# Kernel optimization log

Measured on AMD Instinct MI355X. Metric: run time of the kernel, lower is better.

Reference implementation:

```python
import jax, jax.numpy as jnp
import numpy as np

N, M, E = 100000, 500, 300000
XS, GS, OUT, HEADS = 100, 100, 100, 2
SLOPE = 0.2
EPS = 1e-12


def l2norm(x, axis):
    n = jnp.linalg.norm(x, axis=axis, keepdims=True)
    return x / jnp.maximum(n, EPS)


def gat_layer(h_ijk, ends, n, W, att):
    # W: [heads*out, in_dim] (no bias); att: [1, heads, out]
    heads, out = att.shape[1], att.shape[2]
    c = (h_ijk @ W.T).reshape(-1, heads, out)               # [E, H, D]
    a = jnp.sum(att * c, axis=2, keepdims=True)             # [E, H, 1]
    e = jnp.exp(-jax.nn.leaky_relu(a, SLOPE))
    denom = jax.ops.segment_sum(e, ends, num_segments=n)    # [n, H, 1]
    alpha = e / denom[ends]                                 # segment softmax (dropout=eval/identity)
    h = jax.ops.segment_sum(alpha * c, ends, num_segments=n)  # [n, H, D]
    h = jax.nn.elu(h)
    h = l2norm(h, axis=2)
    return h.reshape(n, heads * out)


def merge_layer(h_in, h_out, Wi, bi, Wo, bo, Wl, bl):
    hi = h_in @ Wi.T + bi
    ho = h_out @ Wo.T + bo
    lam = jax.nn.sigmoid(jnp.concatenate([hi, ho], axis=1) @ Wl.T + bl)
    h = lam * hi + (1.0 - lam) * ho
    return l2norm(jax.nn.elu(h), axis=1)


def setup_inputs() -> dict:
    key = jax.random.key(0)
    ks = jax.random.split(key, 24)
    D = HEADS * OUT  # 200
    in1 = 2 * XS + GS   # 300
    in2 = 3 * D         # 600
    s = 0.05
    return {
        'edge_idx': jax.random.randint(ks[0], (2, E), 0, N),
        'edge_type': jax.random.randint(ks[1], (E,), 0, M),
        'path_idx': jax.random.randint(ks[2], (2, 8), 0, N),
        'path_type': jax.random.randint(ks[3], (2, 8), 0, M),
        'use_path': 0,
        'x': jax.random.normal(ks[4], (N, XS), jnp.float32),
        'g': jax.random.normal(ks[5], (M, GS), jnp.float32),
        'W_in1': s * jax.random.normal(ks[6], (D, in1), jnp.float32),
        'att_in1': s * jax.random.normal(ks[7], (1, HEADS, OUT), jnp.float32),
        'W_out1': s * jax.random.normal(ks[8], (D, in1), jnp.float32),
        'att_out1': s * jax.random.normal(ks[9], (1, HEADS, OUT), jnp.float32),
        'Wi1': s * jax.random.normal(ks[10], (D, D), jnp.float32), 'bi1': jnp.zeros((D,), jnp.float32),
        'Wo1': s * jax.random.normal(ks[11], (D, D), jnp.float32), 'bo1': jnp.zeros((D,), jnp.float32),
        'Wl1': s * jax.random.normal(ks[12], (1, 2 * D), jnp.float32), 'bl1': jnp.zeros((1,), jnp.float32),
        'Wr': s * jax.random.normal(ks[13], (D, GS), jnp.float32), 'br': jnp.zeros((D,), jnp.float32),
        'Wf': s * jax.random.normal(ks[14], (D, in1), jnp.float32), 'bf': jnp.zeros((D,), jnp.float32),
        'W_in2': s * jax.random.normal(ks[15], (D, in2), jnp.float32),
        'att_in2': s * jax.random.normal(ks[16], (1, 1, D), jnp.float32),
        'W_out2': s * jax.random.normal(ks[17], (D, in2), jnp.float32),
        'att_out2': s * jax.random.normal(ks[18], (1, 1, D), jnp.float32),
        'Wi2': s * jax.random.normal(ks[19], (D, D), jnp.float32), 'bi2': jnp.zeros((D,), jnp.float32),
        'Wo2': s * jax.random.normal(ks[20], (D, D), jnp.float32), 'bo2': jnp.zeros((D,), jnp.float32),
        'Wl2': s * jax.random.normal(ks[21], (1, 2 * D), jnp.float32), 'bl2': jnp.zeros((1,), jnp.float32),
        'W_ent': s * jax.random.normal(ks[22], (D, XS), jnp.float32),
    }


def reference(edge_idx, edge_type, path_idx, path_type, use_path, x, g,
              W_in1, att_in1, W_out1, att_out1, Wi1, bi1, Wo1, bo1, Wl1, bl1,
              Wr, br, Wf, bf,
              W_in2, att_in2, W_out2, att_out2, Wi2, bi2, Wo2, bo2, Wl2, bl2,
              W_ent):
    n, m = x.shape[0], g.shape[0]
    x = l2norm(x, axis=1)  # x_initial is renormalized each forward
    row, col = edge_idx[0], edge_idx[1]
    # hop 1: gather-concat per-edge features [E, 2*XS+GS]
    h_ijk = jnp.concatenate([x[row], x[col], g[edge_type]], axis=1)
    h_in = gat_layer(h_ijk, col, n, W_in1, att_in1)
    h_out = gat_layer(h_ijk, row, n, W_out1, att_out1)
    h = merge_layer(h_in, h_out, Wi1, bi1, Wo1, bo1, Wl1, bl1)
    # relation layer
    g_edges = jax.ops.segment_sum(h_ijk, edge_type, num_segments=m)
    g_edges = jax.nn.elu(l2norm(g_edges, axis=1))
    g_prime = (g @ Wr.T + br) + (g_edges @ Wf.T + bf)
    # hop 2
    h_ijk2 = jnp.concatenate([h[row], h[col], g_prime[edge_type]], axis=1)
    h_in2 = gat_layer(h_ijk2, col, n, W_in2, att_in2)
    h_out2 = gat_layer(h_ijk2, row, n, W_out2, att_out2)
    h = merge_layer(h_in2, h_out2, Wi2, bi2, Wo2, bo2, Wl2, bl2)
    # entity residual layer
    h_prime = x @ W_ent.T + h
    return h_prime
```

## Files before the change

### kernel.cpp

```cpp
#include <hip/hip_runtime.h>
#include <cstddef>
#include <cstdint>

#define WSLOPE 0.2f
#define WEPS 1e-12f

typedef __attribute__((ext_vector_type(8))) short bf16x8;
typedef __attribute__((ext_vector_type(4))) float f32x4;

__device__ __forceinline__ float waveSum(float v) {
#pragma unroll
    for (int off = 32; off > 0; off >>= 1) v += __shfl_xor(v, off, 64);
    return v;
}
__device__ __forceinline__ float rowSum16(float v) {
#pragma unroll
    for (int off = 8; off > 0; off >>= 1) v += __shfl_xor(v, off, 64);
    return v;
}
__device__ __forceinline__ float eluf(float v) { return v > 0.f ? v : expm1f(v); }
__device__ __forceinline__ short f2bf(float f) {
    union { float f; uint32_t u; } v; v.f = f;
    uint32_t r = v.u + 0x7FFF + ((v.u >> 16) & 1);
    return (short)(r >> 16);
}
__device__ __forceinline__ float bf2f(short s) {
    union { uint32_t u; float f; } v; v.u = ((uint32_t)(uint16_t)s) << 16;
    return v.f;
}

__global__ void k_nodeprep(const float* __restrict__ x, float* __restrict__ invn,
                           short* __restrict__ xnb,
                           const float* __restrict__ wai, const float* __restrict__ wao,
                           float* __restrict__ rdi, float* __restrict__ cdi,
                           float* __restrict__ rdo, float* __restrict__ cdo, int N) {
    int wid = blockIdx.x * 4 + (threadIdx.x >> 6);
    int lane = threadIdx.x & 63;
    if (wid >= N) return;
    const float* p = x + (size_t)wid * 100;
    float a0 = p[lane];
    float a1 = (lane < 36) ? p[lane + 64] : 0.f;
    float ss = waveSum(a0 * a0 + a1 * a1);
    float inv = 1.f / fmaxf(sqrtf(ss), WEPS);
    if (lane == 0) invn[wid] = inv;
    float f0 = a0 * inv, f1 = a1 * inv;
    short* xb = xnb + (size_t)wid * 112;
    xb[lane] = f2bf(f0);
    if (lane < 36) xb[64 + lane] = f2bf(f1);
    else if (lane < 48) xb[64 + lane] = 0;
#pragma unroll
    for (int h = 0; h < 2; ++h) {
        const float* wi = wai + h * 300;
        const float* wo = wao + h * 300;
        float ri = f0 * wi[lane] + f1 * wi[lane + 64];
        float ci = f0 * wi[100 + lane] + f1 * wi[100 + lane + 64];
        float ro = f0 * wo[lane] + f1 * wo[lane + 64];
        float co = f0 * wo[100 + lane] + f1 * wo[100 + lane + 64];
        ri = waveSum(ri); ci = waveSum(ci); ro = waveSum(ro); co = waveSum(co);
        if (lane == 0) { rdi[wid * 2 + h] = ri; cdi[wid * 2 + h] = ci; rdo[wid * 2 + h] = ro; cdo[wid * 2 + h] = co; }
    }
}

__global__ void k_gprep(const float* __restrict__ g, short* __restrict__ gbf,
                        short* __restrict__ gcomb,
                        const float* __restrict__ wai, const float* __restrict__ wao,
                        float* __restrict__ gdi, float* __restrict__ gdo, int M) {
    int m = blockIdx.x * 4 + (threadIdx.x >> 6);
    int lane = threadIdx.x & 63;
    if (m >= M) return;
    const float* gm = g + (size_t)m * 100;
    float v0 = gm[lane];
    float v1 = (lane < 36) ? gm[lane + 64] : 0.f;
    short b0 = f2bf(v0), b1 = (lane < 36) ? f2bf(v1) : (short)0;
    short* gb = gbf + (size_t)m * 112;
    gb[lane] = b0;
    if (lane < 48) gb[64 + lane] = (lane < 36) ? b1 : (short)0;
    short* gc = gcomb + (size_t)m * 416;
    gc[lane] = b0;
    if (lane < 48) gc[64 + lane] = (lane < 36) ? b1 : (short)0;
    float s0 = v0 * wai[200 + lane];
    float s1 = v0 * wai[500 + lane];
    float s2 = v0 * wao[200 + lane];
    float s3 = v0 * wao[500 + lane];
    if (lane < 36) {
        s0 += v1 * wai[264 + lane]; s1 += v1 * wai[564 + lane];
        s2 += v1 * wao[264 + lane]; s3 += v1 * wao[564 + lane];
    }
    s0 = waveSum(s0); s1 = waveSum(s1); s2 = waveSum(s2); s3 = waveSum(s3);
    if (lane == 0) { gdi[m * 2] = s0; gdi[m * 2 + 1] = s1; gdo[m * 2] = s2; gdo[m * 2 + 1] = s3; }
}

__global__ void k_count(const int* __restrict__ keys, int* __restrict__ cnt, int n) {
    int i = blockIdx.x * 256 + threadIdx.x;
    if (i < n) atomicAdd(&cnt[keys[i]], 1);
}

#define SCAN_CHUNK 2048
__global__ void k_blocksum(const int* __restrict__ cnt, int* __restrict__ bsum, int n) {
    __shared__ int sh[256];
    int b = blockIdx.x, t = threadIdx.x;
    int base = b * SCAN_CHUNK;
    int s = 0;
    for (int i = t; i < SCAN_CHUNK; i += 256) { int idx = base + i; if (idx < n) s += cnt[idx]; }
    sh[t] = s; __syncthreads();
    for (int off = 128; off > 0; off >>= 1) { if (t < off) sh[t] += sh[t + off]; __syncthreads(); }
    if (t == 0) bsum[b] = sh[0];
}

__global__ void k_scanwrite(const int* __restrict__ cnt, const int* __restrict__ bsum,
                            int* __restrict__ offs, int* __restrict__ cur, int n, int nb) {
    __shared__ int sh[256];
    __shared__ int sbase;
    int b = blockIdx.x, t = threadIdx.x;
    if (t == 0) { int s = 0; for (int i = 0; i < b; ++i) s += bsum[i]; sbase = s; }
    __syncthreads();
    int base = b * SCAN_CHUNK;
    int loc[8]; int ts = 0;
#pragma unroll
    for (int i = 0; i < 8; ++i) { int idx = base + t * 8 + i; int v = (idx < n) ? cnt[idx] : 0; loc[i] = ts; ts += v; }
    sh[t] = ts; __syncthreads();
    for (int off = 1; off < 256; off <<= 1) {
        int v = (t >= off) ? sh[t - off] : 0;
        __syncthreads();
        sh[t] += v;
        __syncthreads();
    }
    int excl = (t == 0) ? 0 : sh[t - 1];
    int gbase = sbase + excl;
#pragma unroll
    for (int i = 0; i < 8; ++i) {
        int idx = base + t * 8 + i;
        if (idx < n) { offs[idx] = gbase + loc[i]; cur[idx] = gbase + loc[i]; }
    }
    if (b == nb - 1 && t == 255) offs[n] = sbase + sh[255];
}

__global__ void k_scatter3(const int* __restrict__ keys, const int* __restrict__ other,
                           const int* __restrict__ et, int* __restrict__ cur,
                           int* __restrict__ nbrS, int* __restrict__ etS,
                           int* __restrict__ keyS, int n) {
    int i = blockIdx.x * 256 + threadIdx.x;
    if (i < n) {
        int p = atomicAdd(&cur[keys[i]], 1);
        nbrS[p] = other[i];
        etS[p] = et[i];
        keyS[p] = keys[i];
    }
}

__global__ void k_scatter2(const int* __restrict__ keys, int* __restrict__ cur,
                           int* __restrict__ rs, int* __restrict__ cs,
                           const int* __restrict__ row, const int* __restrict__ col, int n) {
    int i = blockIdx.x * 256 + threadIdx.x;
    if (i < n) {
        int p = atomicAdd(&cur[keys[i]], 1);
        rs[p] = row[i];
        cs[p] = col[i];
    }
}

__global__ void k_watt(const float* __restrict__ att, const float* __restrict__ W,
                       float* __restrict__ wa, int H, int DH, int K) {
    int id = blockIdx.x * 256 + threadIdx.x;
    if (id >= H * K) return;
    int h = id / K, k = id % K;
    float s = 0.f;
    for (int j = 0; j < DH; ++j) s += att[h * DH + j] * W[(size_t)(h * DH + j) * K + k];
    wa[id] = s;
}

__global__ void k_ew2(const int* __restrict__ nbi, const int* __restrict__ kyi,
                      const int* __restrict__ eti,
                      const int* __restrict__ nbo, const int* __restrict__ kyo,
                      const int* __restrict__ eto,
                      const float* __restrict__ rdi, const float* __restrict__ cdi,
                      const float* __restrict__ rdo, const float* __restrict__ cdo,
                      const float* __restrict__ gdi, const float* __restrict__ gdo,
                      float* __restrict__ ewi, float* __restrict__ ewo, int E, int H) {
    int id = blockIdx.x * 256 + threadIdx.x;
    int tot = E * H;
    if (id >= 2 * tot) return;
    if (id < tot) {
        int p = id / H, h = id - p * H;
        float a = rdi[nbi[p] * H + h] + cdi[kyi[p] * H + h] + gdi[eti[p] * H + h];
        float lr = a > 0.f ? a : WSLOPE * a;
        ewi[id] = expf(-lr);
    } else {
        int id2 = id - tot;
        int p = id2 / H, h = id2 - p * H;
        float a = cdo[nbo[p] * H + h] + rdo[kyo[p] * H + h] + gdo[eto[p] * H + h];
        float lr = a > 0.f ? a : WSLOPE * a;
        ewo[id2] = expf(-lr);
    }
}

template<bool HOP2>
__global__ void k_agg(const int* __restrict__ offs, const int* __restrict__ nbrS,
                      const int* __restrict__ etS, const float* __restrict__ ewS,
                      const short* __restrict__ featB, const short* __restrict__ gB,
                      short* __restrict__ A, int n0, int n1) {
    constexpr int H = HOP2 ? 1 : 2;
    constexpr int LDA = 448;
    constexpr int FW = HOP2 ? 224 : 112;
    constexpr int GW = HOP2 ? 224 : 112;
    int node = n0 + blockIdx.x * 4 + (threadIdx.x >> 6);
    int lane = threadIdx.x & 63;
    if (node >= n1) return;
    int o = offs[node];
    int deg = offs[node + 1] - o;
    float va[7];
#pragma unroll
    for (int m = 0; m < 7; ++m) va[m] = 0.f;
    if (deg > 0) {
        float s0 = 0.f, s1 = 0.f;
        for (int i = lane; i < deg; i += 64) {
            s0 += ewS[(size_t)(o + i) * H];
            if (H == 2) s1 += ewS[(size_t)(o + i) * H + 1];
        }
        s0 = waveSum(s0);
        float rd0 = 1.f / s0, rd1 = rd0;
        if (H == 2) { s1 = waveSum(s1); rd1 = 1.f / s1; }
        for (int j = 0; j < deg; ++j) {
            float a0 = ewS[(size_t)(o + j) * H] * rd0;
            float a1 = (H == 2) ? ewS[(size_t)(o + j) * H + 1] * rd1 : a0;
            int nbr = nbrS[o + j];
            int et = etS[o + j];
            const short* fr = featB + (size_t)nbr * FW;
            const short* gr = gB + (size_t)et * GW;
            if (!HOP2) {
#pragma unroll
                for (int m = 0; m < 7; ++m) {
                    int d = lane + m * 64;
                    if (d < 100) va[m] += a0 * bf2f(fr[d]);
                    else if (d < 200) va[m] += a1 * bf2f(fr[d - 100]);
                    else if (d < 300) va[m] += a0 * bf2f(gr[d - 200]);
                    else if (d < 400) va[m] += a1 * bf2f(gr[d - 300]);
                }
            } else {
#pragma unroll
                for (int m = 0; m < 7; ++m) {
                    int d = lane + m * 64;
                    if (d < 200) va[m] += a0 * bf2f(fr[d]);
                    else if (d < 424) va[m] += a0 * bf2f(gr[d - 200]);
                }
            }
        }
    }
    size_t rb = (size_t)(node - n0);
    short* Ar = A + rb * LDA;
    if (!HOP2) {
#pragma unroll
        for (int m = 0; m < 7; ++m) {
            int d = lane + m * 64;
            if (d < 400) {
                int col = d < 100 ? d : (d < 200 ? d + 12 : (d < 300 ? d + 24 : d + 36));
                Ar[col] = f2bf(va[m]);
            }
        }
        if (lane < 48) { int q = lane / 12; int rm = lane - q * 12; Ar[q * 112 + 100 + rm] = 0; }
    } else {
#pragma unroll
        for (int m = 0; m < 7; ++m) {
            int d = lane + m * 64;
            if (d < 424) Ar[d < 200 ? d : d + 24] = f2bf(va[m]);
        }
        if (lane < 24) Ar[200 + lane] = 0;
    }
}

template<int KS_S, int H>
__launch_bounds__(256)
__global__ void k_mgemm_post(const short* __restrict__ A, const short* __restrict__ Wb,
                             const short* __restrict__ selfB, int selfLD,
                             const int* __restrict__ offs,
                             short* __restrict__ post, int rows) {
    constexpr int KS_A = 14;
    constexpr int LDW = (KS_A + KS_S) * 32;
    const int t = threadIdx.x;
    const int wv = t >> 6, l = t & 63;
    const int lhi = l >> 4, llo = l & 15;
    const int rbase = blockIdx.x * 64 + wv * 16;
    const int ra = rbase + llo;
    const int deg = (ra < rows) ? (offs[ra + 1] - offs[ra]) : 0;
    f32x4 acc[13];
#pragma unroll
    for (int j = 0; j < 13; ++j) acc[j] = f32x4{0.f, 0.f, 0.f, 0.f};
    const short* arow = A + (size_t)ra * 448 + lhi * 8;
#pragma unroll
    for (int kt = 0; kt < KS_A; ++kt) {
        bf16x8 a = *(const bf16x8*)(arow + kt * 32);
#pragma unroll
        for (int j = 0; j < 13; ++j) {
            bf16x8 b = *(const bf16x8*)(Wb + (size_t)(j * 16 + llo) * LDW + kt * 32 + lhi * 8);
            acc[j] = __builtin_amdgcn_mfma_f32_16x16x32_bf16(a, b, acc[j], 0, 0, 0);
        }
    }
    const short* srow = selfB + (size_t)ra * selfLD + lhi * 8;
#pragma unroll
    for (int kt = 0; kt < KS_S; ++kt) {
        bf16x8 a;
        if (deg > 0) a = *(const bf16x8*)(srow + kt * 32);
        else a = bf16x8{0, 0, 0, 0, 0, 0, 0, 0};
#pragma unroll
        for (int j = 0; j < 13; ++j) {
            bf16x8 b = *(const bf16x8*)(Wb + (size_t)(j * 16 + llo) * LDW + (KS_A + kt) * 32 + lhi * 8);
            acc[j] = __builtin_amdgcn_mfma_f32_16x16x32_bf16(a, b, acc[j], 0, 0, 0);
        }
    }
    const int r0 = rbase + lhi * 4;
#pragma unroll
    for (int e = 0; e < 4; ++e) {
        int r = r0 + e;
        if (r >= rows) continue;
        float v[13];
        float s0 = 0.f, s1 = 0.f;
#pragma unroll
        for (int j = 0; j < 13; ++j) {
            int d = j * 16 + llo;
            if (d < 200) {
                float xv = eluf(acc[j][e]);
                v[j] = xv;
                if (H == 1 || d < 100) s0 += xv * xv; else s1 += xv * xv;
            }
        }
        s0 = rowSum16(s0);
        float inv0 = 1.f / fmaxf(sqrtf(s0), WEPS);
        float inv1 = inv0;
        if (H == 2) { s1 = rowSum16(s1); inv1 = 1.f / fmaxf(sqrtf(s1), WEPS); }
        short* pr = post + (size_t)r * 224;
#pragma unroll
        for (int j = 0; j < 13; ++j) {
            int d = j * 16 + llo;
            if (d < 200) pr[d] = f2bf(v[j] * ((H == 2 && d >= 100) ? inv1 : inv0));
        }
    }
}

template<bool HOP1>
__launch_bounds__(512)
__global__ void k_mergemm2(const short* __restrict__ pA, const short* __restrict__ pB,
                           const short* __restrict__ Wi, const short* __restrict__ Wo,
                           const float* __restrict__ bi, const float* __restrict__ bo,
                           const float* __restrict__ Wl, const float* __restrict__ bl,
                           const short* __restrict__ xnb, const short* __restrict__ Went,
                           float* __restrict__ outf, short* __restrict__ h1b,
                           const float* __restrict__ wa2i, const float* __restrict__ wa2o,
                           float* __restrict__ rdi, float* __restrict__ cdi,
                           float* __restrict__ rdo, float* __restrict__ cdo,
                           int rows) {
    __shared__ float lpS[2][64];
    __shared__ float ssS[2][64];
    __shared__ float dotS[2][64][4];
    const int t = threadIdx.x;
    const int wvAll = t >> 6;
    const int rg = wvAll >> 1;
    const int half = wvAll & 1;
    const int l = t & 63;
    const int lhi = l >> 4, llo = l & 15;
    const int jbase = half * 7;
    const int rbase = blockIdx.x * 64 + rg * 16;
    f32x4 accA[7], accB[7];
#pragma unroll
    for (int j = 0; j < 7; ++j) { accA[j] = f32x4{0.f, 0.f, 0.f, 0.f}; accB[j] = f32x4{0.f, 0.f, 0.f, 0.f}; }
    const short* pa = pA + (size_t)(rbase + llo) * 224 + lhi * 8;
    const short* pb = pB + (size_t)(rbase + llo) * 224 + lhi * 8;
#pragma unroll
    for (int kt = 0; kt < 7; ++kt) {
        bf16x8 a1 = *(const bf16x8*)(pa + kt * 32);
        bf16x8 a2 = *(const bf16x8*)(pb + kt * 32);
#pragma unroll
        for (int j = 0; j < 7; ++j) {
            if (jbase + j < 13) {
                bf16x8 b1 = *(const bf16x8*)(Wi + (size_t)((jbase + j) * 16 + llo) * 224 + kt * 32 + lhi * 8);
                accA[j] = __builtin_amdgcn_mfma_f32_16x16x32_bf16(a1, b1, accA[j], 0, 0, 0);
                bf16x8 b2 = *(const bf16x8*)(Wo + (size_t)((jbase + j) * 16 + llo) * 224 + kt * 32 + lhi * 8);
                accB[j] = __builtin_amdgcn_mfma_f32_16x16x32_bf16(a2, b2, accB[j], 0, 0, 0);
            }
        }
    }
    f32x4 accR[7];
    if (!HOP1) {
#pragma unroll
        for (int j = 0; j < 7; ++j) accR[j] = f32x4{0.f, 0.f, 0.f, 0.f};
        const short* xr = xnb + (size_t)(rbase + llo) * 112 + lhi * 8;
#pragma unroll
        for (int kt = 0; kt < 4; ++kt) {
            bf16x8 a = *(const bf16x8*)(xr + kt * 32);
#pragma unroll
            for (int j = 0; j < 7; ++j) {
                if (jbase + j < 13) {
                    bf16x8 b = *(const bf16x8*)(Went + (size_t)((jbase + j) * 16 + llo) * 128 + kt * 32 + lhi * 8);
                    accR[j] = __builtin_amdgcn_mfma_f32_16x16x32_bf16(a, b, accR[j], 0, 0, 0);
                }
            }
        }
    }
    const int r0 = rbase + lhi * 4;
    const int rrb = rg * 16 + lhi * 4;
    float blv = bl[0];
#pragma unroll
    for (int e = 0; e < 4; ++e) {
        float lp = 0.f;
#pragma unroll
        for (int j = 0; j < 7; ++j) {
            int d = (jbase + j) * 16 + llo;
            if (jbase + j < 13 && d < 200)
                lp += Wl[d] * (accA[j][e] + bi[d]) + Wl[200 + d] * (accB[j][e] + bo[d]);
        }
        lp = rowSum16(lp);
        if (llo == 0) lpS[half][rrb + e] = lp;
    }
    __syncthreads();
    float lamAll[4];
#pragma unroll
    for (int e = 0; e < 4; ++e) {
        float lam = 1.f / (1.f + expf(-(lpS[0][rrb + e] + lpS[1][rrb + e] + blv)));
        lamAll[e] = lam;
        float ss = 0.f;
#pragma unroll
        for (int j = 0; j < 7; ++j) {
            int d = (jbase + j) * 16 + llo;
            if (jbase + j < 13 && d < 200) {
                float vi = accA[j][e] + bi[d];
                float vo = accB[j][e] + bo[d];
                float hv = eluf(lam * vi + (1.f - lam) * vo);
                ss += hv * hv;
            }
        }
        ss = rowSum16(ss);
        if (llo == 0) ssS[half][rrb + e] = ss;
    }
    __syncthreads();
#pragma unroll
    for (int e = 0; e < 4; ++e) {
        int r = r0 + e;
        if (r >= rows) continue;
        float inv = 1.f / fmaxf(sqrtf(ssS[0][rrb + e] + ssS[1][rrb + e]), WEPS);
        float lam = lamAll[e];
        float ri = 0.f, ci = 0.f, ro = 0.f, co = 0.f;
#pragma unroll
        for (int j = 0; j < 7; ++j) {
            if (jbase + j >= 13) continue;
            int d = (jbase + j) * 16 + llo;
            if (d < 200) {
                float vi = accA[j][e] + bi[d];
                float vo = accB[j][e] + bo[d];
                float val = eluf(lam * vi + (1.f - lam) * vo) * inv;
                if (HOP1) {
                    h1b[(size_t)r * 224 + d] = f2bf(val);
                    ri += val * wa2i[d]; ci += val * wa2i[200 + d];
                    ro += val * wa2o[d]; co += val * wa2o[200 + d];
                } else {
                    outf[(size_t)r * 200 + d] = val + accR[j][e];
                }
            } else if (HOP1) {
                h1b[(size_t)r * 224 + d] = 0;
            }
        }
        if (HOP1) {
            if (half) h1b[(size_t)r * 224 + 208 + llo] = 0;
            ri = rowSum16(ri); ci = rowSum16(ci); ro = rowSum16(ro); co = rowSum16(co);
            if (llo == 0) {
                dotS[half][rrb + e][0] = ri; dotS[half][rrb + e][1] = ci;
                dotS[half][rrb + e][2] = ro; dotS[half][rrb + e][3] = co;
            }
        }
    }
    if (HOP1) {
        __syncthreads();
        if (half == 0 && llo == 0) {
#pragma unroll
            for (int e = 0; e < 4; ++e) {
                int r = r0 + e;
                if (r < rows) {
                    rdi[r] = dotS[0][rrb + e][0] + dotS[1][rrb + e][0];
                    cdi[r] = dotS[0][rrb + e][1] + dotS[1][rrb + e][1];
                    rdo[r] = dotS[0][rrb + e][2] + dotS[1][rrb + e][2];
                    cdo[r] = dotS[0][rrb + e][3] + dotS[1][rrb + e][3];
                }
            }
        }
    }
}

__launch_bounds__(256)
__global__ void k_mgemm_rel(const short* __restrict__ A, const short* __restrict__ Wb,
                            const float* __restrict__ brf,
                            short* __restrict__ gout, const float* __restrict__ wai,
                            const float* __restrict__ wao,
                            float* __restrict__ gdi, float* __restrict__ gdo, int rows) {
    constexpr int KSTEPS = 13, LDW = KSTEPS * 32;
    const int t = threadIdx.x;
    const int wv = t >> 6, l = t & 63;
    const int lhi = l >> 4, llo = l & 15;
    const int rbase = blockIdx.x * 64 + wv * 16;
    f32x4 acc[13];
#pragma unroll
    for (int j = 0; j < 13; ++j) acc[j] = f32x4{0.f, 0.f, 0.f, 0.f};
    const short* arow = A + (size_t)(rbase + llo) * 416 + lhi * 8;
#pragma unroll
    for (int kt = 0; kt < KSTEPS; ++kt) {
        bf16x8 a = *(const bf16x8*)(arow + kt * 32);
#pragma unroll
        for (int j = 0; j < 13; ++j) {
            bf16x8 b = *(const bf16x8*)(Wb + (size_t)(j * 16 + llo) * LDW + kt * 32 + lhi * 8);
            acc[j] = __builtin_amdgcn_mfma_f32_16x16x32_bf16(a, b, acc[j], 0, 0, 0);
        }
    }
    const int r0 = rbase + lhi * 4;
#pragma unroll
    for (int e = 0; e < 4; ++e) {
        int r = r0 + e;
        if (r >= rows) continue;
        short* pr = gout + (size_t)r * 224;
        float gi = 0.f, go = 0.f;
#pragma unroll
        for (int j = 0; j < 13; ++j) {
            int d = j * 16 + llo;
            if (d < 200) {
                float val = acc[j][e] + brf[d];
                pr[d] = f2bf(val);
                gi += val * wai[400 + d];
                go += val * wao[400 + d];
            } else {
                pr[d] = 0;
            }
        }
        pr[208 + llo] = 0;
        gi = rowSum16(gi); go = rowSum16(go);
        if (llo == 0) { gdi[r] = gi; gdo[r] = go; }
    }
}

__global__ void k_prepw(const float* __restrict__ W, int ldW, int koff, int Klen, int span,
                        int mode, short* __restrict__ Wb, int ldWb, int dst) {
    int id = blockIdx.x * 256 + threadIdx.x;
    int tot = 208 * span;
    if (id >= tot) return;
    int d = id / span, k = id - d * span;
    float v = 0.f;
    if (d < 200) {
        if (mode == 0) { if (k < Klen) v = W[(size_t)d * ldW + koff + k]; }
        else { int h = d / 100; int kk = k - h * 112; if (kk >= 0 && kk < Klen) v = W[(size_t)d * ldW + koff + kk]; }
    }
    Wb[(size_t)d * ldWb + dst + k] = f2bf(v);
}

__global__ void k_prepwrf(const float* __restrict__ Wr, const float* __restrict__ Wf,
                          short* __restrict__ Wb) {
    int id = blockIdx.x * 256 + threadIdx.x;
    if (id >= 208 * 416) return;
    int d = id / 416, k = id - d * 416;
    float v = 0.f;
    if (d < 200) {
        if (k < 100) v = Wr[(size_t)d * 100 + k];
        else if (k >= 112 && k < 412) v = Wf[(size_t)d * 300 + (k - 112)];
    }
    Wb[id] = f2bf(v);
}

__global__ void k_brf(const float* __restrict__ br, const float* __restrict__ bf,
                      float* __restrict__ brf) {
    int d = threadIdx.x;
    if (d < 200) brf[d] = br[d] + bf[d];
}

__global__ void k_gedges_b(const int* __restrict__ rsT, const int* __restrict__ csT,
                           const int* __restrict__ offsT,
                           const short* __restrict__ xnb,
                           const short* __restrict__ gbf, short* __restrict__ gcomb, int M) {
    __shared__ float red[6];
    int m = blockIdx.x, t = threadIdx.x;
    int o = offsT[m];
    int deg = offsT[m + 1] - o;
    float acc = 0.f;
    if (t < 128) {
        int d = t; bool ok = d < 100;
        for (int i = 0; i < deg; ++i) {
            int r = rsT[o + i];
            if (ok) acc += bf2f(xnb[(size_t)r * 112 + d]);
        }
    } else if (t < 256) {
        int d = t - 128; bool ok = d < 100;
        for (int i = 0; i < deg; ++i) {
            int c = csT[o + i];
            if (ok) acc += bf2f(xnb[(size_t)c * 112 + d]);
        }
    } else {
        int d = t - 256;
        if (d < 100) acc = (float)deg * bf2f(gbf[(size_t)m * 112 + d]);
    }
    float sq = waveSum(acc * acc);
    if ((t & 63) == 0) red[t >> 6] = sq;
    __syncthreads();
    float s2 = red[0] + red[1] + red[2] + red[3] + red[4] + red[5];
    float inv = 1.f / fmaxf(sqrtf(s2), WEPS);
    short* orow = gcomb + (size_t)m * 416 + 112;
    if (t < 128) {
        if (t < 100) orow[t] = f2bf(eluf(acc * inv));
    } else if (t < 256) {
        int d = t - 128;
        if (d < 100) orow[100 + d] = f2bf(eluf(acc * inv));
    } else {
        int d = t - 256;
        if (d < 100) orow[200 + d] = f2bf(eluf(acc * inv));
        else if (d < 104) orow[200 + d] = 0;
    }
}

extern "C" void kernel_launch(void* const* d_in, const int* in_sizes, int n_in,
                              void* d_out, int out_size, void* d_ws, size_t ws_size,
                              hipStream_t stream) {
    const int* eidx   = (const int*)d_in[0];
    const int* etype  = (const int*)d_in[1];
    const float* x    = (const float*)d_in[5];
    const float* g    = (const float*)d_in[6];
    const float* W_in1  = (const float*)d_in[7];
    const float* att_in1 = (const float*)d_in[8];
    const float* W_out1 = (const float*)d_in[9];
    const float* att_out1 = (const float*)d_in[10];
    const float* Wi1 = (const float*)d_in[11]; const float* bi1 = (const float*)d_in[12];
    const float* Wo1 = (const float*)d_in[13]; const float* bo1 = (const float*)d_in[14];
    const float* Wl1 = (const float*)d_in[15]; const float* bl1 = (const float*)d_in[16];
    const float* Wr  = (const float*)d_in[17]; const float* br  = (const float*)d_in[18];
    const float* Wf  = (const float*)d_in[19]; const float* bf  = (const float*)d_in[20];
    const float* W_in2  = (const float*)d_in[21]; const float* att_in2 = (const float*)d_in[22];
    const float* W_out2 = (const float*)d_in[23]; const float* att_out2 = (const float*)d_in[24];
    const float* Wi2 = (const float*)d_in[25]; const float* bi2 = (const float*)d_in[26];
    const float* Wo2 = (const float*)d_in[27]; const float* bo2 = (const float*)d_in[28];
    const float* Wl2 = (const float*)d_in[29]; const float* bl2 = (const float*)d_in[30];
    const float* W_ent = (const float*)d_in[31];

    const int E = in_sizes[1];
    const int N = in_sizes[5] / 100;
    const int M = in_sizes[6] / 100;
    const int Mr = (M + 63) & ~63;
    float* out = (float*)d_out;
    const int* row = eidx;
    const int* col = eidx + E;

    char* w = (char*)d_ws;
    size_t off_b = 0;
    auto alloc = [&](size_t bytes) -> void* {
        void* p = w + off_b;
        off_b += (bytes + 255) & ~(size_t)255;
        return p;
    };
    float* invn  = (float*)alloc((size_t)N * 4);
    short* h1_bf = (short*)alloc((size_t)(N + 64) * 224 * 2);
    short* xn_bf = (short*)alloc((size_t)(N + 64) * 112 * 2);
    short* g_bf  = (short*)alloc((size_t)M * 112 * 2);
    short* gp_bf = (short*)alloc((size_t)Mr * 224 * 2);
    int* offs_in = (int*)alloc((size_t)(N + 1) * 4);
    int* offs_out= (int*)alloc((size_t)(N + 1) * 4);
    int* offsT   = (int*)alloc((size_t)(M + 1) * 4);
    int* nbrS_in = (int*)alloc((size_t)E * 4);
    int* etS_in  = (int*)alloc((size_t)E * 4);
    int* keyS_in = (int*)alloc((size_t)E * 4);
    int* nbrS_out= (int*)alloc((size_t)E * 4);
    int* etS_out = (int*)alloc((size_t)E * 4);
    int* keyS_out= (int*)alloc((size_t)E * 4);
    int* rsT     = (int*)alloc((size_t)E * 4);
    int* csT     = (int*)alloc((size_t)E * 4);
    int* cnt     = (int*)alloc((size_t)N * 4);
    int* cur     = (int*)alloc((size_t)N * 4);
    int* bsum    = (int*)alloc((size_t)64 * 4);
    float* wa1_in = (float*)alloc((size_t)640 * 4);
    float* wa1_out= (float*)alloc((size_t)640 * 4);
    float* wa2_in = (float*)alloc((size_t)640 * 4);
    float* wa2_out= (float*)alloc((size_t)640 * 4);
    float* rdot_in = (float*)alloc((size_t)N * 2 * 4);
    float* cdot_in = (float*)alloc((size_t)N * 2 * 4);
    float* rdot_out= (float*)alloc((size_t)N * 2 * 4);
    float* cdot_out= (float*)alloc((size_t)N * 2 * 4);
    float* gdot_in = (float*)alloc((size_t)M * 2 * 4);
    float* gdot_out= (float*)alloc((size_t)M * 2 * 4);
    float* ewS_in  = (float*)alloc((size_t)E * 2 * 4);
    float* ewS_out = (float*)alloc((size_t)E * 2 * 4);
    short* gcomb   = (short*)alloc((size_t)Mr * 416 * 2);
    short* Wc_in1  = (short*)alloc((size_t)208 * 576 * 2);
    short* Wc_out1 = (short*)alloc((size_t)208 * 576 * 2);
    short* Wc_in2  = (short*)alloc((size_t)208 * 672 * 2);
    short* Wc_out2 = (short*)alloc((size_t)208 * 672 * 2);
    short* Wm_i1   = (short*)alloc((size_t)208 * 224 * 2);
    short* Wm_o1   = (short*)alloc((size_t)208 * 224 * 2);
    short* Wm_i2   = (short*)alloc((size_t)208 * 224 * 2);
    short* Wm_o2   = (short*)alloc((size_t)208 * 224 * 2);
    short* Wb_ent  = (short*)alloc((size_t)208 * 128 * 2);
    short* Wrf_b   = (short*)alloc((size_t)208 * 416 * 2);
    float* brf     = (float*)alloc((size_t)200 * 4);

    if (off_b >= ws_size) return;
    size_t rem = ws_size - off_b;
    long long Cll = (long long)(rem / 1920);
    long long Nr64 = ((long long)N + 63) & ~63LL;
    int C = (int)(Cll > Nr64 ? Nr64 : Cll);
    C &= ~63;
    if (C < 64) return;
    short* Ac    = (short*)alloc((size_t)C * 448 * 2);
    short* postA = (short*)alloc((size_t)C * 224 * 2);
    short* postB = (short*)alloc((size_t)C * 224 * 2);
    if (off_b > ws_size) return;

    const int gE = (E + 255) / 256;
    const int gN4 = (N + 3) / 4;
    const int gM4 = (M + 3) / 4;
    const int gM64 = (M + 63) / 64;

    hipMemsetAsync(postA, 0, (size_t)C * 224 * 2, stream);
    hipMemsetAsync(postB, 0, (size_t)C * 224 * 2, stream);
    hipMemsetAsync(xn_bf + (size_t)N * 112, 0, (size_t)64 * 112 * 2, stream);
    hipMemsetAsync(h1_bf + (size_t)N * 224, 0, (size_t)64 * 224 * 2, stream);

    auto gsp = [](int span) { return (208 * span + 255) / 256; };
    k_prepw<<<gsp(224), 256, 0, stream>>>(W_in1, 300, 0, 100, 224, 1, Wc_in1, 576, 0);
    k_prepw<<<gsp(224), 256, 0, stream>>>(W_in1, 300, 200, 100, 224, 1, Wc_in1, 576, 224);
    k_prepw<<<gsp(128), 256, 0, stream>>>(W_in1, 300, 100, 100, 128, 0, Wc_in1, 576, 448);
    k_prepw<<<gsp(224), 256, 0, stream>>>(W_out1, 300, 100, 100, 224, 1, Wc_out1, 576, 0);
    k_prepw<<<gsp(224), 256, 0, stream>>>(W_out1, 300, 200, 100, 224, 1, Wc_out1, 576, 224);
    k_prepw<<<gsp(128), 256, 0, stream>>>(W_out1, 300, 0, 100, 128, 0, Wc_out1, 576, 448);
    k_prepw<<<gsp(224), 256, 0, stream>>>(W_in2, 600, 0, 200, 224, 0, Wc_in2, 672, 0);
    k_prepw<<<gsp(224), 256, 0, stream>>>(W_in2, 600, 400, 200, 224, 0, Wc_in2, 672, 224);
    k_prepw<<<gsp(224), 256, 0, stream>>>(W_in2, 600, 200, 200, 224, 0, Wc_in2, 672, 448);
    k_prepw<<<gsp(224), 256, 0, stream>>>(W_out2, 600, 200, 200, 224, 0, Wc_out2, 672, 0);
    k_prepw<<<gsp(224), 256, 0, stream>>>(W_out2, 600, 400, 200, 224, 0, Wc_out2, 672, 224);
    k_prepw<<<gsp(224), 256, 0, stream>>>(W_out2, 600, 0, 200, 224, 0, Wc_out2, 672, 448);
    k_prepw<<<gsp(224), 256, 0, stream>>>(Wi1, 200, 0, 200, 224, 0, Wm_i1, 224, 0);
    k_prepw<<<gsp(224), 256, 0, stream>>>(Wo1, 200, 0, 200, 224, 0, Wm_o1, 224, 0);
    k_prepw<<<gsp(224), 256, 0, stream>>>(Wi2, 200, 0, 200, 224, 0, Wm_i2, 224, 0);
    k_prepw<<<gsp(224), 256, 0, stream>>>(Wo2, 200, 0, 200, 224, 0, Wm_o2, 224, 0);
    k_prepw<<<gsp(128), 256, 0, stream>>>(W_ent, 100, 0, 100, 128, 0, Wb_ent, 128, 0);
    k_prepwrf<<<gsp(416), 256, 0, stream>>>(Wr, Wf, Wrf_b);
    k_brf<<<1, 256, 0, stream>>>(br, bf, brf);

    int nbN = (N + SCAN_CHUNK - 1) / SCAN_CHUNK;
    int nbM = (M + SCAN_CHUNK - 1) / SCAN_CHUNK;
    hipMemsetAsync(cnt, 0, (size_t)N * 4, stream);
    k_count<<<gE, 256, 0, stream>>>(col, cnt, E);
    k_blocksum<<<nbN, 256, 0, stream>>>(cnt, bsum, N);
    k_scanwrite<<<nbN, 256, 0, stream>>>(cnt, bsum, offs_in, cur, N, nbN);
    k_scatter3<<<gE, 256, 0, stream>>>(col, row, etype, cur, nbrS_in, etS_in, keyS_in, E);

    hipMemsetAsync(cnt, 0, (size_t)N * 4, stream);
    k_count<<<gE, 256, 0, stream>>>(row, cnt, E);
    k_blocksum<<<nbN, 256, 0, stream>>>(cnt, bsum, N);
    k_scanwrite<<<nbN, 256, 0, stream>>>(cnt, bsum, offs_out, cur, N, nbN);
    k_scatter3<<<gE, 256, 0, stream>>>(row, col, etype, cur, nbrS_out, etS_out, keyS_out, E);

    hipMemsetAsync(cnt, 0, (size_t)M * 4, stream);
    k_count<<<gE, 256, 0, stream>>>(etype, cnt, E);
    k_blocksum<<<nbM, 256, 0, stream>>>(cnt, bsum, M);
    k_scanwrite<<<nbM, 256, 0, stream>>>(cnt, bsum, offsT, cur, M, nbM);
    k_scatter2<<<gE, 256, 0, stream>>>(etype, cur, rsT, csT, row, col, E);

    k_watt<<<(600 + 255) / 256, 256, 0, stream>>>(att_in1, W_in1, wa1_in, 2, 100, 300);
    k_watt<<<(600 + 255) / 256, 256, 0, stream>>>(att_out1, W_out1, wa1_out, 2, 100, 300);
    k_watt<<<(600 + 255) / 256, 256, 0, stream>>>(att_in2, W_in2, wa2_in, 1, 200, 600);
    k_watt<<<(600 + 255) / 256, 256, 0, stream>>>(att_out2, W_out2, wa2_out, 1, 200, 600);

    k_nodeprep<<<gN4, 256, 0, stream>>>(x, invn, xn_bf, wa1_in, wa1_out,
                                        rdot_in, cdot_in, rdot_out, cdot_out, N);
    k_gprep<<<gM4, 256, 0, stream>>>(g, g_bf, gcomb, wa1_in, wa1_out, gdot_in, gdot_out, M);
    k_ew2<<<(2 * E * 2 + 255) / 256, 256, 0, stream>>>(nbrS_in, keyS_in, etS_in,
                                                       nbrS_out, keyS_out, etS_out,
                                                       rdot_in, cdot_in, rdot_out, cdot_out,
                                                       gdot_in, gdot_out, ewS_in, ewS_out, E, 2);

    for (int n0 = 0; n0 < N; n0 += C) {
        int rows = (N - n0 < C) ? (N - n0) : C;
        int n1 = n0 + rows;
        int ga = (rows + 3) / 4;
        int gb = (rows + 63) / 64;
        k_agg<false><<<ga, 256, 0, stream>>>(offs_in, nbrS_in, etS_in, ewS_in, xn_bf, g_bf, Ac, n0, n1);
        k_mgemm_post<4, 2><<<gb, 256, 0, stream>>>(Ac, Wc_in1, xn_bf + (size_t)n0 * 112, 112,
                                                   offs_in + n0, postA, rows);
        k_agg<false><<<ga, 256, 0, stream>>>(offs_out, nbrS_out, etS_out, ewS_out, xn_bf, g_bf, Ac, n0, n1);
        k_mgemm_post<4, 2><<<gb, 256, 0, stream>>>(Ac, Wc_out1, xn_bf + (size_t)n0 * 112, 112,
                                                   offs_out + n0, postB, rows);
        k_mergemm2<true><<<gb, 512, 0, stream>>>(postA, postB, Wm_i1, Wm_o1, bi1, bo1, Wl1, bl1,
                                                 nullptr, nullptr,
                                                 nullptr, h1_bf + (size_t)n0 * 224,
                                                 wa2_in, wa2_out,
                                                 rdot_in + n0, cdot_in + n0,
                                                 rdot_out + n0, cdot_out + n0, rows);
    }

    k_gedges_b<<<M, 384, 0, stream>>>(rsT, csT, offsT, xn_bf, g_bf, gcomb, M);
    k_mgemm_rel<<<gM64, 256, 0, stream>>>(gcomb, Wrf_b, brf, gp_bf, wa2_in, wa2_out, gdot_in, gdot_out, M);

    k_ew2<<<(2 * E + 255) / 256, 256, 0, stream>>>(nbrS_in, keyS_in, etS_in,
                                                   nbrS_out, keyS_out, etS_out,
                                                   rdot_in, cdot_in, rdot_out, cdot_out,
                                                   gdot_in, gdot_out, ewS_in, ewS_out, E, 1);

    for (int n0 = 0; n0 < N; n0 += C) {
        int rows = (N - n0 < C) ? (N - n0) : C;
        int n1 = n0 + rows;
        int ga = (rows + 3) / 4;
        int gb = (rows + 63) / 64;
        k_agg<true><<<ga, 256, 0, stream>>>(offs_in, nbrS_in, etS_in, ewS_in, h1_bf, gp_bf, Ac, n0, n1);
        k_mgemm_post<7, 1><<<gb, 256, 0, stream>>>(Ac, Wc_in2, h1_bf + (size_t)n0 * 224, 224,
                                                   offs_in + n0, postA, rows);
        k_agg<true><<<ga, 256, 0, stream>>>(offs_out, nbrS_out, etS_out, ewS_out, h1_bf, gp_bf, Ac, n0, n1);
        k_mgemm_post<7, 1><<<gb, 256, 0, stream>>>(Ac, Wc_out2, h1_bf + (size_t)n0 * 224, 224,
                                                   offs_out + n0, postB, rows);
        k_mergemm2<false><<<gb, 512, 0, stream>>>(postA, postB, Wm_i2, Wm_o2, bi2, bo2, Wl2, bl2,
                                                  xn_bf + (size_t)n0 * 112, Wb_ent,
                                                  out + (size_t)n0 * 200, nullptr,
                                                  nullptr, nullptr,
                                                  nullptr, nullptr, nullptr, nullptr, rows);
    }
}
```

Before: 2.513 ms.

## Pack per-node attention dots into float4 and fuse in/out aggregation kernels

Per-node attention dot products (row/col, in/out, per head) are packed into f32x4 records so each edge-weight thread gathers one 16-byte vector per endpoint instead of several scattered floats; relation dots become f32x2. The edge-weight kernel is split into hop-specific versions with shift/mask indexing instead of integer division. The in- and out-direction aggregation kernels are merged into one launch that writes two separate A buffers, which halves launch count and needs twice the A scratch, shrinking the chunk size C.

```diff
diff --git a/kernel.cpp b/kernel.cpp
--- a/kernel.cpp
+++ b/kernel.cpp
@@ -7,6 +7,7 @@
 
 typedef __attribute__((ext_vector_type(8))) short bf16x8;
 typedef __attribute__((ext_vector_type(4))) float f32x4;
+typedef __attribute__((ext_vector_type(2))) float f32x2;
 
 __device__ __forceinline__ float waveSum(float v) {
 #pragma unroll
@@ -29,11 +30,9 @@
     return v.f;
 }
 
-__global__ void k_nodeprep(const float* __restrict__ x, float* __restrict__ invn,
-                           short* __restrict__ xnb,
+__global__ void k_nodeprep(const float* __restrict__ x, short* __restrict__ xnb,
                            const float* __restrict__ wai, const float* __restrict__ wao,
-                           float* __restrict__ rdi, float* __restrict__ cdi,
-                           float* __restrict__ rdo, float* __restrict__ cdo, int N) {
+                           f32x4* __restrict__ ndi, f32x4* __restrict__ ndo, int N) {
     int wid = blockIdx.x * 4 + (threadIdx.x >> 6);
     int lane = threadIdx.x & 63;
     if (wid >= N) return;
@@ -42,12 +41,12 @@
     float a1 = (lane < 36) ? p[lane + 64] : 0.f;
     float ss = waveSum(a0 * a0 + a1 * a1);
     float inv = 1.f / fmaxf(sqrtf(ss), WEPS);
-    if (lane == 0) invn[wid] = inv;
     float f0 = a0 * inv, f1 = a1 * inv;
     short* xb = xnb + (size_t)wid * 112;
     xb[lane] = f2bf(f0);
     if (lane < 36) xb[64 + lane] = f2bf(f1);
     else if (lane < 48) xb[64 + lane] = 0;
+    float rI[2], cI[2], rO[2], cO[2];
 #pragma unroll
     for (int h = 0; h < 2; ++h) {
         const float* wi = wai + h * 300;
@@ -56,8 +55,11 @@
         float ci = f0 * wi[100 + lane] + f1 * wi[100 + lane + 64];
         float ro = f0 * wo[lane] + f1 * wo[lane + 64];
         float co = f0 * wo[100 + lane] + f1 * wo[100 + lane + 64];
-        ri = waveSum(ri); ci = waveSum(ci); ro = waveSum(ro); co = waveSum(co);
-        if (lane == 0) { rdi[wid * 2 + h] = ri; cdi[wid * 2 + h] = ci; rdo[wid * 2 + h] = ro; cdo[wid * 2 + h] = co; }
+        rI[h] = waveSum(ri); cI[h] = waveSum(ci); rO[h] = waveSum(ro); cO[h] = waveSum(co);
+    }
+    if (lane == 0) {
+        ndi[wid] = f32x4{rI[0], rI[1], cI[0], cI[1]};
+        ndo[wid] = f32x4{rO[0], rO[1], cO[0], cO[1]};
     }
 }
 
@@ -169,36 +171,65 @@
     wa[id] = s;
 }
 
-__global__ void k_ew2(const int* __restrict__ nbi, const int* __restrict__ kyi,
-                      const int* __restrict__ eti,
-                      const int* __restrict__ nbo, const int* __restrict__ kyo,
-                      const int* __restrict__ eto,
-                      const float* __restrict__ rdi, const float* __restrict__ cdi,
-                      const float* __restrict__ rdo, const float* __restrict__ cdo,
-                      const float* __restrict__ gdi, const float* __restrict__ gdo,
-                      float* __restrict__ ewi, float* __restrict__ ewo, int E, int H) {
+__global__ void k_ewh1(const int* __restrict__ nbi, const int* __restrict__ kyi,
+                       const int* __restrict__ eti,
+                       const int* __restrict__ nbo, const int* __restrict__ kyo,
+                       const int* __restrict__ eto,
+                       const f32x4* __restrict__ ndi, const f32x4* __restrict__ ndo,
+                       const float* __restrict__ gdi, const float* __restrict__ gdo,
+                       float* __restrict__ ewi, float* __restrict__ ewo, int E) {
     int id = blockIdx.x * 256 + threadIdx.x;
-    int tot = E * H;
+    int tot = E * 2;
     if (id >= 2 * tot) return;
     if (id < tot) {
-        int p = id / H, h = id - p * H;
-        float a = rdi[nbi[p] * H + h] + cdi[kyi[p] * H + h] + gdi[eti[p] * H + h];
+        int p = id >> 1, h = id & 1;
+        f32x4 n1 = ndi[nbi[p]];
+        f32x4 n2 = ndi[kyi[p]];
+        float a = (h ? n1.y : n1.x) + (h ? n2.w : n2.z) + gdi[eti[p] * 2 + h];
         float lr = a > 0.f ? a : WSLOPE * a;
         ewi[id] = expf(-lr);
     } else {
         int id2 = id - tot;
-        int p = id2 / H, h = id2 - p * H;
-        float a = cdo[nbo[p] * H + h] + rdo[kyo[p] * H + h] + gdo[eto[p] * H + h];
+        int p = id2 >> 1, h = id2 & 1;
+        f32x4 n1 = ndo[nbo[p]];
+        f32x4 n2 = ndo[kyo[p]];
+        float a = (h ? n1.w : n1.z) + (h ? n2.y : n2.x) + gdo[eto[p] * 2 + h];
         float lr = a > 0.f ? a : WSLOPE * a;
         ewo[id2] = expf(-lr);
     }
 }
 
+__global__ void k_ewh2(const int* __restrict__ nbi, const int* __restrict__ kyi,
+                       const int* __restrict__ eti,
+                       const int* __restrict__ nbo, const int* __restrict__ kyo,
+                       const int* __restrict__ eto,
+                       const f32x4* __restrict__ nd2, const f32x2* __restrict__ gd2,
+                       float* __restrict__ ewi, float* __restrict__ ewo, int E) {
+    int id = blockIdx.x * 256 + threadIdx.x;
+    if (id >= 2 * E) return;
+    if (id < E) {
+        f32x4 n1 = nd2[nbi[id]];
+        f32x4 n2 = nd2[kyi[id]];
+        float a = n1.x + n2.y + gd2[eti[id]].x;
+        float lr = a > 0.f ? a : WSLOPE * a;
+        ewi[id] = expf(-lr);
+    } else {
+        int p = id - E;
+        f32x4 n1 = nd2[nbo[p]];
+        f32x4 n2 = nd2[kyo[p]];
+        float a = n1.w + n2.z + gd2[eto[p]].y;
+        float lr = a > 0.f ? a : WSLOPE * a;
+        ewo[p] = expf(-lr);
+    }
+}
+
 template<bool HOP2>
-__global__ void k_agg(const int* __restrict__ offs, const int* __restrict__ nbrS,
-                      const int* __restrict__ etS, const float* __restrict__ ewS,
-                      const short* __restrict__ featB, const short* __restrict__ gB,
-                      short* __restrict__ A, int n0, int n1) {
+__global__ void k_agg2(const int* __restrict__ offsI, const int* __restrict__ nbrI,
+                       const int* __restrict__ etI, const float* __restrict__ ewI,
+                       const int* __restrict__ offsO, const int* __restrict__ nbrO,
+                       const int* __restrict__ etO, const float* __restrict__ ewO,
+                       const short* __restrict__ featB, const short* __restrict__ gB,
+                       short* __restrict__ A0, short* __restrict__ A1, int n0, int n1) {
     constexpr int H = HOP2 ? 1 : 2;
     constexpr int LDA = 448;
     constexpr int FW = HOP2 ? 224 : 112;
@@ -206,65 +237,73 @@
     int node = n0 + blockIdx.x * 4 + (threadIdx.x >> 6);
     int lane = threadIdx.x & 63;
     if (node >= n1) return;
-    int o = offs[node];
-    int deg = offs[node + 1] - o;
-    float va[7];
-#pragma unroll
-    for (int m = 0; m < 7; ++m) va[m] = 0.f;
-    if (deg > 0) {
-        float s0 = 0.f, s1 = 0.f;
-        for (int i = lane; i < deg; i += 64) {
-            s0 += ewS[(size_t)(o + i) * H];
-            if (H == 2) s1 += ewS[(size_t)(o + i) * H + 1];
-        }
-        s0 = waveSum(s0);
-        float rd0 = 1.f / s0, rd1 = rd0;
-        if (H == 2) { s1 = waveSum(s1); rd1 = 1.f / s1; }
-        for (int j = 0; j < deg; ++j) {
-            float a0 = ewS[(size_t)(o + j) * H] * rd0;
-            float a1 = (H == 2) ? ewS[(size_t)(o + j) * H + 1] * rd1 : a0;
-            int nbr = nbrS[o + j];
-            int et = etS[o + j];
-            const short* fr = featB + (size_t)nbr * FW;
-            const short* gr = gB + (size_t)et * GW;
-            if (!HOP2) {
-#pragma unroll
-                for (int m = 0; m < 7; ++m) {
-                    int d = lane + m * 64;
-                    if (d < 100) va[m] += a0 * bf2f(fr[d]);
-                    else if (d < 200) va[m] += a1 * bf2f(fr[d - 100]);
-                    else if (d < 300) va[m] += a0 * bf2f(gr[d - 200]);
-                    else if (d < 400) va[m] += a1 * bf2f(gr[d - 300]);
+#pragma unroll 1
+    for (int dir = 0; dir < 2; ++dir) {
+        const int* offs = dir ? offsO : offsI;
+        const int* nbrS = dir ? nbrO : nbrI;
+        const int* etS  = dir ? etO  : etI;
+        const float* ewS = dir ? ewO : ewI;
+        short* A = dir ? A1 : A0;
+        int o = offs[node];
+        int deg = offs[node + 1] - o;
+        float va[7];
+#pragma unroll
+        for (int m = 0; m < 7; ++m) va[m] = 0.f;
+        if (deg > 0) {
+            float s0 = 0.f, s1 = 0.f;
+            for (int i = lane; i < deg; i += 64) {
+                s0 += ewS[(size_t)(o + i) * H];
+                if (H == 2) s1 += ewS[(size_t)(o + i) * H + 1];
+            }
+            s0 = waveSum(s0);
+            float rd0 = 1.f / s0, rd1 = rd0;
+            if (H == 2) { s1 = waveSum(s1); rd1 = 1.f / s1; }
+            for (int j = 0; j < deg; ++j) {
+                float a0 = ewS[(size_t)(o + j) * H] * rd0;
+                float a1 = (H == 2) ? ewS[(size_t)(o + j) * H + 1] * rd1 : a0;
+                int nbr = nbrS[o + j];
+                int et = etS[o + j];
+                const short* fr = featB + (size_t)nbr * FW;
+                const short* gr = gB + (size_t)et * GW;
+                if (!HOP2) {
+#pragma unroll
+                    for (int m = 0; m < 7; ++m) {
+                        int d = lane + m * 64;
+                        if (d < 100) va[m] += a0 * bf2f(fr[d]);
+                        else if (d < 200) va[m] += a1 * bf2f(fr[d - 100]);
+                        else if (d < 300) va[m] += a0 * bf2f(gr[d - 200]);
+                        else if (d < 400) va[m] += a1 * bf2f(gr[d - 300]);
+                    }
+                } else {
+#pragma unroll
+                    for (int m = 0; m < 7; ++m) {
+                        int d = lane + m * 64;
+                        if (d < 200) va[m] += a0 * bf2f(fr[d]);
+                        else if (d < 424) va[m] += a0 * bf2f(gr[d - 200]);
+                    }
                 }
-            } else {
-#pragma unroll
-                for (int m = 0; m < 7; ++m) {
-                    int d = lane + m * 64;
-                    if (d < 200) va[m] += a0 * bf2f(fr[d]);
-                    else if (d < 424) va[m] += a0 * bf2f(gr[d - 200]);
+            }
+        }
+        size_t rb = (size_t)(node - n0);
+        short* Ar = A + rb * LDA;
+        if (!HOP2) {
+#pragma unroll
+            for (int m = 0; m < 7; ++m) {
+                int d = lane + m * 64;
+                if (d < 400) {
+                    int col = d < 100 ? d : (d < 200 ? d + 12 : (d < 300 ? d + 24 : d + 36));
+                    Ar[col] = f2bf(va[m]);
                 }
             }
-        }
-    }
-    size_t rb = (size_t)(node - n0);
-    short* Ar = A + rb * LDA;
-    if (!HOP2) {
-#pragma unroll
-        for (int m = 0; m < 7; ++m) {
-            int d = lane + m * 64;
-            if (d < 400) {
-                int col = d < 100 ? d : (d < 200 ? d + 12 : (d < 300 ? d + 24 : d + 36));
-                Ar[col] = f2bf(va[m]);
-            }
-        }
-        if (lane < 48) { int q = lane / 12; int rm = lane - q * 12; Ar[q * 112 + 100 + rm] = 0; }
-    } else {
-#pragma unroll
-        for (int m = 0; m < 7; ++m) {
-            int d = lane + m * 64;
-            if (d < 424) Ar[d < 200 ? d : d + 24] = f2bf(va[m]);
-        }
-        if (lane < 24) Ar[200 + lane] = 0;
+            if (lane < 48) { int q = lane / 12; int rm = lane - q * 12; Ar[q * 112 + 100 + rm] = 0; }
+        } else {
+#pragma unroll
+            for (int m = 0; m < 7; ++m) {
+                int d = lane + m * 64;
+                if (d < 424) Ar[d < 200 ? d : d + 24] = f2bf(va[m]);
+            }
+            if (lane < 24) Ar[200 + lane] = 0;
+        }
     }
 }
 
@@ -345,8 +384,7 @@
                            const short* __restrict__ xnb, const short* __restrict__ Went,
                            float* __restrict__ outf, short* __restrict__ h1b,
                            const float* __restrict__ wa2i, const float* __restrict__ wa2o,
-                           float* __restrict__ rdi, float* __restrict__ cdi,
-                           float* __restrict__ rdo, float* __restrict__ cdo,
+                           f32x4* __restrict__ nd2,
                            int rows) {
     __shared__ float lpS[2][64];
     __shared__ float ssS[2][64];
@@ -473,10 +511,10 @@
             for (int e = 0; e < 4; ++e) {
                 int r = r0 + e;
                 if (r < rows) {
-                    rdi[r] = dotS[0][rrb + e][0] + dotS[1][rrb + e][0];
-                    cdi[r] = dotS[0][rrb + e][1] + dotS[1][rrb + e][1];
-                    rdo[r] = dotS[0][rrb + e][2] + dotS[1][rrb + e][2];
-                    cdo[r] = dotS[0][rrb + e][3] + dotS[1][rrb + e][3];
+                    nd2[r] = f32x4{dotS[0][rrb + e][0] + dotS[1][rrb + e][0],
+                                   dotS[0][rrb + e][1] + dotS[1][rrb + e][1],
+                                   dotS[0][rrb + e][2] + dotS[1][rrb + e][2],
+                                   dotS[0][rrb + e][3] + dotS[1][rrb + e][3]};
                 }
             }
         }
@@ -488,7 +526,7 @@
                             const float* __restrict__ brf,
                             short* __restrict__ gout, const float* __restrict__ wai,
                             const float* __restrict__ wao,
-                            float* __restrict__ gdi, float* __restrict__ gdo, int rows) {
+                            f32x2* __restrict__ gd2, int rows) {
     constexpr int KSTEPS = 13, LDW = KSTEPS * 32;
     const int t = threadIdx.x;
     const int wv = t >> 6, l = t & 63;
@@ -528,7 +566,7 @@
         }
         pr[208 + llo] = 0;
         gi = rowSum16(gi); go = rowSum16(go);
-        if (llo == 0) { gdi[r] = gi; gdo[r] = go; }
+        if (llo == 0) gd2[r] = f32x2{gi, go};
     }
 }
 
@@ -646,7 +684,6 @@
         off_b += (bytes + 255) & ~(size_t)255;
         return p;
     };
-    float* invn  = (float*)alloc((size_t)N * 4);
     short* h1_bf = (short*)alloc((size_t)(N + 64) * 224 * 2);
     short* xn_bf = (short*)alloc((size_t)(N + 64) * 112 * 2);
     short* g_bf  = (short*)alloc((size_t)M * 112 * 2);
@@ -669,12 +706,12 @@
     float* wa1_out= (float*)alloc((size_t)640 * 4);
     float* wa2_in = (float*)alloc((size_t)640 * 4);
     float* wa2_out= (float*)alloc((size_t)640 * 4);
-    float* rdot_in = (float*)alloc((size_t)N * 2 * 4);
-    float* cdot_in = (float*)alloc((size_t)N * 2 * 4);
-    float* rdot_out= (float*)alloc((size_t)N * 2 * 4);
-    float* cdot_out= (float*)alloc((size_t)N * 2 * 4);
+    f32x4* nd1i  = (f32x4*)alloc((size_t)N * 16);
+    f32x4* nd1o  = (f32x4*)alloc((size_t)N * 16);
+    f32x4* nd2   = (f32x4*)alloc((size_t)N * 16);
     float* gdot_in = (float*)alloc((size_t)M * 2 * 4);
     float* gdot_out= (float*)alloc((size_t)M * 2 * 4);
+    f32x2* gd2   = (f32x2*)alloc((size_t)M * 8);
     float* ewS_in  = (float*)alloc((size_t)E * 2 * 4);
     float* ewS_out = (float*)alloc((size_t)E * 2 * 4);
     short* gcomb   = (short*)alloc((size_t)Mr * 416 * 2);
@@ -692,12 +729,13 @@
 
     if (off_b >= ws_size) return;
     size_t rem = ws_size - off_b;
-    long long Cll = (long long)(rem / 1920);
+    long long Cll = (long long)(rem / 2816);
     long long Nr64 = ((long long)N + 63) & ~63LL;
     int C = (int)(Cll > Nr64 ? Nr64 : Cll);
     C &= ~63;
     if (C < 64) return;
-    short* Ac    = (short*)alloc((size_t)C * 448 * 2);
+    short* Ac0   = (short*)alloc((size_t)C * 448 * 2);
+    short* Ac1   = (short*)alloc((size_t)C * 448 * 2);
     short* postA = (short*)alloc((size_t)C * 224 * 2);
     short* postB = (short*)alloc((size_t)C * 224 * 2);
     if (off_b > ws_size) return;
@@ -758,56 +796,53 @@
     k_watt<<<(600 + 255) / 256, 256, 0, stream>>>(att_in2, W_in2, wa2_in, 1, 200, 600);
     k_watt<<<(600 + 255) / 256, 256, 0, stream>>>(att_out2, W_out2, wa2_out, 1, 200, 600);
 
-    k_nodeprep<<<gN4, 256, 0, stream>>>(x, invn, xn_bf, wa1_in, wa1_out,
-                                        rdot_in, cdot_in, rdot_out, cdot_out, N);
+    k_nodeprep<<<gN4, 256, 0, stream>>>(x, xn_bf, wa1_in, wa1_out, nd1i, nd1o, N);
     k_gprep<<<gM4, 256, 0, stream>>>(g, g_bf, gcomb, wa1_in, wa1_out, gdot_in, gdot_out, M);
-    k_ew2<<<(2 * E * 2 + 255) / 256, 256, 0, stream>>>(nbrS_in, keyS_in, etS_in,
-                                                       nbrS_out, keyS_out, etS_out,
-                                                       rdot_in, cdot_in, rdot_out, cdot_out,
-                                                       gdot_in, gdot_out, ewS_in, ewS_out, E, 2);
+    k_ewh1<<<(2 * E * 2 + 255) / 256, 256, 0, stream>>>(nbrS_in, keyS_in, etS_in,
+                                                        nbrS_out, keyS_out, etS_out,
+                                                        nd1i, nd1o, gdot_in, gdot_out,
+                                                        ewS_in, ewS_out, E);
 
     for (int n0 = 0; n0 < N; n0 += C) {
         int rows = (N - n0 < C) ? (N - n0) : C;
         int n1 = n0 + rows;
         int ga = (rows + 3) / 4;
         int gb = (rows + 63) / 64;
-        k_agg<false><<<ga, 256, 0, stream>>>(offs_in, nbrS_in, etS_in, ewS_in, xn_bf, g_bf, Ac, n0, n1);
-        k_mgemm_post<4, 2><<<gb, 256, 0, stream>>>(Ac, Wc_in1, xn_bf + (size_t)n0 * 112, 112,
+        k_agg2<false><<<ga, 256, 0, stream>>>(offs_in, nbrS_in, etS_in, ewS_in,
+                                              offs_out, nbrS_out, etS_out, ewS_out,
+                                              xn_bf, g_bf, Ac0, Ac1, n0, n1);
+        k_mgemm_post<4, 2><<<gb, 256, 0, stream>>>(Ac0, Wc_in1, xn_bf + (size_t)n0 * 112, 112,
                                                    offs_in + n0, postA, rows);
-        k_agg<false><<<ga, 256, 0, stream>>>(offs_out, nbrS_out, etS_out, ewS_out, xn_bf, g_bf, Ac, n0, n1);
-        k_mgemm_post<4, 2><<<gb, 256, 0, stream>>>(Ac, Wc_out1, xn_bf + (size_t)n0 * 112, 112,
+        k_mgemm_post<4, 2><<<gb, 256, 0, stream>>>(Ac1, Wc_out1, xn_bf + (size_t)n0 * 112, 112,
                                                    offs_out + n0, postB, rows);
         k_mergemm2<true><<<gb, 512, 0, stream>>>(postA, postB, Wm_i1, Wm_o1, bi1, bo1, Wl1, bl1,
                                                  nullptr, nullptr,
                                                  nullptr, h1_bf + (size_t)n0 * 224,
-                                                 wa2_in, wa2_out,
-                                                 rdot_in + n0, cdot_in + n0,
-                                                 rdot_out + n0, cdot_out + n0, rows);
+                                                 wa2_in, wa2_out, nd2 + n0, rows);
     }
 
     k_gedges_b<<<M, 384, 0, stream>>>(rsT, csT, offsT, xn_bf, g_bf, gcomb, M);
-    k_mgemm_rel<<<gM64, 256, 0, stream>>>(gcomb, Wrf_b, brf, gp_bf, wa2_in, wa2_out, gdot_in, gdot_out, M);
-
-    k_ew2<<<(2 * E + 255) / 256, 256, 0, stream>>>(nbrS_in, keyS_in, etS_in,
-                                                   nbrS_out, keyS_out, etS_out,
-                                                   rdot_in, cdot_in, rdot_out, cdot_out,
-                                                   gdot_in, gdot_out, ewS_in, ewS_out, E, 1);
+    k_mgemm_rel<<<gM64, 256, 0, stream>>>(gcomb, Wrf_b, brf, gp_bf, wa2_in, wa2_out, gd2, M);
+
+    k_ewh2<<<(2 * E + 255) / 256, 256, 0, stream>>>(nbrS_in, keyS_in, etS_in,
+                                                    nbrS_out, keyS_out, etS_out,
+                                                    nd2, gd2, ewS_in, ewS_out, E);
 
     for (int n0 = 0; n0 < N; n0 += C) {
         int rows = (N - n0 < C) ? (N - n0) : C;
         int n1 = n0 + rows;
         int ga = (rows + 3) / 4;
         int gb = (rows + 63) / 64;
-        k_agg<true><<<ga, 256, 0, stream>>>(offs_in, nbrS_in, etS_in, ewS_in, h1_bf, gp_bf, Ac, n0, n1);
-        k_mgemm_post<7, 1><<<gb, 256, 0, stream>>>(Ac, Wc_in2, h1_bf + (size_t)n0 * 224, 224,
+        k_agg2<true><<<ga, 256, 0, stream>>>(offs_in, nbrS_in, etS_in, ewS_in,
+                                             offs_out, nbrS_out, etS_out, ewS_out,
+                                             h1_bf, gp_bf, Ac0, Ac1, n0, n1);
+        k_mgemm_post<7, 1><<<gb, 256, 0, stream>>>(Ac0, Wc_in2, h1_bf + (size_t)n0 * 224, 224,
                                                    offs_in + n0, postA, rows);
-        k_agg<true><<<ga, 256, 0, stream>>>(offs_out, nbrS_out, etS_out, ewS_out, h1_bf, gp_bf, Ac, n0, n1);
-        k_mgemm_post<7, 1><<<gb, 256, 0, stream>>>(Ac, Wc_out2, h1_bf + (size_t)n0 * 224, 224,
+        k_mgemm_post<7, 1><<<gb, 256, 0, stream>>>(Ac1, Wc_out2, h1_bf + (size_t)n0 * 224, 224,
                                                    offs_out + n0, postB, rows);
         k_mergemm2<false><<<gb, 512, 0, stream>>>(postA, postB, Wm_i2, Wm_o2, bi2, bo2, Wl2, bl2,
                                                   xn_bf + (size_t)n0 * 112, Wb_ent,
                                                   out + (size_t)n0 * 200, nullptr,
-                                                  nullptr, nullptr,
-                                                  nullptr, nullptr, nullptr, nullptr, rows);
-    }
-}
+                                                  nullptr, nullptr, nullptr, rows);
+    }
+}
```

After: 2.662 ms. 5.9% more time.
